# Optimization experiments

Hardware: AMD Instinct MI355X
Metric: run time of the kernel (lower is better)

## Reference

```python
import jax, jax.numpy as jnp
import numpy as np
from jax import lax

D_MODEL = 1024
D_STATE = 1024  # must equal D_MODEL due to u*B elementwise multiply in selective_scan
D_CONV = 4
BATCH = 4
SEQ = 4096


def setup_inputs() -> dict:
    key = jax.random.key(0)
    ks = jax.random.split(key, 12)
    s = 0.02
    return {
        "x": jax.random.normal(ks[0], (BATCH, SEQ, D_MODEL), jnp.float32),
        "ln_g": jnp.ones((D_MODEL,), jnp.float32),
        "ln_b": jnp.zeros((D_MODEL,), jnp.float32),
        "w_in": jax.random.normal(ks[1], (2 * D_MODEL, D_MODEL), jnp.float32) * s,
        "b_in": jnp.zeros((2 * D_MODEL,), jnp.float32),
        "w_conv": jax.random.normal(ks[2], (D_MODEL, 1, D_CONV), jnp.float32) * 0.2,
        "b_conv": jnp.zeros((D_MODEL,), jnp.float32),
        "w_delta": jax.random.normal(ks[3], (D_STATE, D_MODEL), jnp.float32) * s,
        "b_delta": jnp.zeros((D_STATE,), jnp.float32),
        "w_B": jax.random.normal(ks[4], (D_STATE, D_MODEL), jnp.float32) * s,
        "b_B": jnp.zeros((D_STATE,), jnp.float32),
        "w_C": jax.random.normal(ks[5], (D_STATE, D_MODEL), jnp.float32) * s,
        "b_C": jnp.zeros((D_STATE,), jnp.float32),
        "w_out": jax.random.normal(ks[6], (D_MODEL, D_MODEL), jnp.float32) * s,
        "b_out": jnp.zeros((D_MODEL,), jnp.float32),
    }


def reference(x, ln_g, ln_b, w_in, b_in, w_conv, b_conv,
              w_delta, b_delta, w_B, b_B, w_C, b_C, w_out, b_out):
    eps = 1e-5
    # LayerNorm
    mu = jnp.mean(x, axis=-1, keepdims=True)
    var = jnp.mean(jnp.square(x - mu), axis=-1, keepdims=True)
    h = (x - mu) * lax.rsqrt(var + eps) * ln_g + ln_b
    # in_proj and chunk
    uv = h @ w_in.T + b_in  # [B, L, 2D]
    u, v = jnp.split(uv, 2, axis=-1)
    # depthwise causal conv1d: torch pads both sides by K-1 then slices [:L] -> left pad only
    K = w_conv.shape[-1]
    u_c = lax.conv_general_dilated(
        u.transpose(0, 2, 1), w_conv, window_strides=(1,),
        padding=[(K - 1, 0)], feature_group_count=u.shape[-1],
        dimension_numbers=("NCH", "OIH", "NCH"))
    u_c = u_c.transpose(0, 2, 1) + b_conv  # [B, L, D]
    # projections
    delta = jax.nn.softplus(u_c @ w_delta.T + b_delta)  # [B, L, N]
    Bm = u_c @ w_B.T + b_B                              # [B, L, N]
    Cm = u_c @ w_C.T + b_C                              # [B, L, N]
    # selective scan: A = -1 broadcast over d_state
    decay = jnp.exp(-delta)        # exp(delta * A)
    inp = u_c * Bm                 # requires d_model == d_state

    def step(hst, t):
        d_t, i_t, c_t = t
        hst = hst * d_t + i_t
        return hst, jnp.sum(hst * c_t, axis=-1)  # [B]

    h0 = jnp.zeros((x.shape[0], Bm.shape[-1]), x.dtype)
    _, ys = lax.scan(step, h0,
                     (decay.transpose(1, 0, 2), inp.transpose(1, 0, 2), Cm.transpose(1, 0, 2)))
    y = ys.T[..., None]            # [B, L, 1]
    y = y * jax.nn.sigmoid(v)      # broadcast to [B, L, D]
    out = y @ w_out.T + b_out
    return x + out
```

## Files before the change

kernel.cpp:

```cpp
#include <hip/hip_runtime.h>
#include <stdint.h>

#define D_MODEL 1024
#define KDIM 1024
#define BATCH 4
#define SEQ 4096
#define MROWS (BATCH*SEQ)
#define CHUNK 64
#define NCHUNK (SEQ/CHUNK)

typedef unsigned short u16;
typedef __attribute__((ext_vector_type(8))) short short8;
typedef __attribute__((ext_vector_type(4))) float f32x4;
typedef __attribute__((ext_vector_type(4))) unsigned short u16x4;

__device__ __forceinline__ u16 f2bf(float f){
  uint32_t b = __builtin_bit_cast(uint32_t, f);
  b += 0x7FFFu + ((b >> 16) & 1u);
  return (u16)(b >> 16);
}
__device__ __forceinline__ float bf2f(u16 u){
  uint32_t b = ((uint32_t)u) << 16;
  return __builtin_bit_cast(float, b);
}

__global__ __launch_bounds__(256) void prep_ln_kernel(
    const float* __restrict__ w_in, const float* __restrict__ w_delta,
    const float* __restrict__ w_B, const float* __restrict__ w_C,
    const float* __restrict__ w_out,
    const float* __restrict__ b_delta, const float* __restrict__ b_B,
    const float* __restrict__ b_C,
    u16* __restrict__ w_in_bf, u16* __restrict__ wcat_bf,
    u16* __restrict__ w_out_bf, float* __restrict__ bcat,
    const float* __restrict__ x, const float* __restrict__ g,
    const float* __restrict__ bb, u16* __restrict__ h){
  if (blockIdx.x >= 6147){
    int row = blockIdx.x - 6147;
    int tid = threadIdx.x, lane = tid & 63, wid = tid >> 6;
    const float* xr = x + (size_t)row * D_MODEL;
    float4 v = *(const float4*)(xr + tid * 4);
    float s  = v.x + v.y + v.z + v.w;
    float s2 = v.x*v.x + v.y*v.y + v.z*v.z + v.w*v.w;
#pragma unroll
    for (int off = 32; off > 0; off >>= 1){ s += __shfl_down(s, off); s2 += __shfl_down(s2, off); }
    __shared__ float red[8];
    if (lane == 0){ red[wid] = s; red[4 + wid] = s2; }
    __syncthreads();
    s  = red[0] + red[1] + red[2] + red[3];
    s2 = red[4] + red[5] + red[6] + red[7];
    float mu  = s * (1.f / D_MODEL);
    float var = s2 * (1.f / D_MODEL) - mu * mu;
    float rs  = rsqrtf(var + 1e-5f);
    int c = tid * 4;
    u16x4 o;
    o.x = f2bf((v.x - mu) * rs * g[c+0] + bb[c+0]);
    o.y = f2bf((v.y - mu) * rs * g[c+1] + bb[c+1]);
    o.z = f2bf((v.z - mu) * rs * g[c+2] + bb[c+2]);
    o.w = f2bf((v.w - mu) * rs * g[c+3] + bb[c+3]);
    *(u16x4*)(h + (size_t)row * D_MODEL + c) = o;
    return;
  }
  int i4 = blockIdx.x * 256 + threadIdx.x;
  const float* src; u16* dst; int off;
  if      (i4 <  524288){ src = w_in;    dst = w_in_bf;           off = i4; }
  else if (i4 <  786432){ src = w_delta; dst = wcat_bf;           off = i4 -  524288; }
  else if (i4 < 1048576){ src = w_B;     dst = wcat_bf + 1048576; off = i4 -  786432; }
  else if (i4 < 1310720){ src = w_C;     dst = wcat_bf + 2097152; off = i4 - 1048576; }
  else if (i4 < 1572864){ src = w_out;   dst = w_out_bf;          off = i4 - 1310720; }
  else {
    int t = i4 - 1572864;
    if      (t < 256){ *(float4*)(bcat +        t*4)        = *(const float4*)(b_delta + t*4); }
    else if (t < 512){ *(float4*)(bcat + 1024 + (t-256)*4)  = *(const float4*)(b_B + (t-256)*4); }
    else if (t < 768){ *(float4*)(bcat + 2048 + (t-512)*4)  = *(const float4*)(b_C + (t-512)*4); }
    return;
  }
  float4 v = *(const float4*)(src + (size_t)off * 4);
  u16x4 o; o.x = f2bf(v.x); o.y = f2bf(v.y); o.z = f2bf(v.z); o.w = f2bf(v.w);
  *(u16x4*)(dst + (size_t)off * 4) = o;
}

#define VMCNT_(N) asm volatile("s_waitcnt vmcnt(" #N ")" ::: "memory")
#define VMCNT(N) VMCNT_(N)

template<int EPI>
__global__ __launch_bounds__(512, 2) void gemm256(
    const u16* __restrict__ A, const u16* __restrict__ W,
    const float* __restrict__ bias,
    u16* __restrict__ outb, float* __restrict__ outf,
    const float* __restrict__ resid, int N){
  __shared__ char lds[131072];
  const int tid = threadIdx.x, wid = tid >> 6, lane = tid & 63;
  const int wm = wid >> 2, wn = wid & 3;
  const int lrow = lane & 15, khi = lane >> 4;

  int nwg = gridDim.x;
  int cpx = nwg >> 3;
  int bid = blockIdx.x;
  int wg = (bid & 7) * cpx + (bid >> 3);
  int ntile = N >> 8;
  int by = wg / ntile, bx = wg % ntile;
  int m0 = by << 8, n0 = bx << 8;

  f32x4 acc[8][4];
  f32x4 zero = {0.f, 0.f, 0.f, 0.f};
#pragma unroll
  for (int i = 0; i < 8; i++)
#pragma unroll
    for (int j = 0; j < 4; j++) acc[i][j] = zero;

  const int xr = ((lrow >> 1) & 3) << 4;
  const int aOff = (wm * 128 + lrow) * 64 + ((khi * 16) ^ xr);
  const int bOff = (wn * 64  + lrow) * 64 + ((khi * 16) ^ xr);

  const int rS = tid >> 2;
  const int cbS = ((tid & 3) * 16) ^ (((rS >> 1) & 3) << 4);
  const u16* gA = A + (size_t)(m0 + rS) * KDIM + (cbS >> 1);
  const u16* gB = W + (size_t)(n0 + rS) * KDIM + (cbS >> 1);

  auto stA = [&](int kt, int bi){
    const u16* g0 = gA + kt;
    unsigned l0 = (unsigned)(bi * 16384 + wid * 1024);
    __builtin_amdgcn_global_load_lds((const __attribute__((address_space(1))) void*)g0,
                                     (__attribute__((address_space(3))) void*)(lds + l0), 16, 0, 0);
    __builtin_amdgcn_global_load_lds((const __attribute__((address_space(1))) void*)(g0 + 128 * KDIM),
                                     (__attribute__((address_space(3))) void*)(lds + l0 + 8192), 16, 0, 0);
  };
  auto stB = [&](int kt, int bi){
    const u16* g0 = gB + kt;
    unsigned l0 = (unsigned)(65536 + bi * 16384 + wid * 1024);
    __builtin_amdgcn_global_load_lds((const __attribute__((address_space(1))) void*)g0,
                                     (__attribute__((address_space(3))) void*)(lds + l0), 16, 0, 0);
    __builtin_amdgcn_global_load_lds((const __attribute__((address_space(1))) void*)(g0 + 128 * KDIM),
                                     (__attribute__((address_space(3))) void*)(lds + l0 + 8192), 16, 0, 0);
  };

#define TILE(BI, STKT, DOSTAGE, WAITC) { \
  const char* pa = lds + (BI) * 16384; \
  const char* pb = lds + 65536 + (BI) * 16384; \
  short8 bfr[4], afr[8]; \
  _Pragma("unroll") \
  for (int nf = 0; nf < 4; nf++) bfr[nf] = *(const short8*)(pb + bOff + nf * 1024); \
  _Pragma("unroll") \
  for (int mi = 0; mi < 8; mi++) afr[mi] = *(const short8*)(pa + aOff + mi * 1024); \
  if (DOSTAGE){ stA((STKT), ((BI) + 3) & 3); stB((STKT), ((BI) + 3) & 3); } \
  __builtin_amdgcn_sched_barrier(0); \
  __builtin_amdgcn_s_setprio(1); \
  _Pragma("unroll") \
  for (int mi = 0; mi < 8; mi++) \
    _Pragma("unroll") \
    for (int nf = 0; nf < 4; nf++) \
      acc[mi][nf] = __builtin_amdgcn_mfma_f32_16x16x32_bf16(afr[mi], bfr[nf], acc[mi][nf], 0, 0, 0); \
  __builtin_amdgcn_s_setprio(0); \
  WAITC; \
  __builtin_amdgcn_s_barrier(); \
}

  stA(0, 0);  stB(0, 0);
  stA(32, 1); stB(32, 1);
  stA(64, 2); stB(64, 2);
  VMCNT(8);
  __builtin_amdgcn_s_barrier();

  for (int kk = 0; kk < 28; kk += 4){
    TILE(0, (kk + 3) << 5, 1, VMCNT(8));
    TILE(1, (kk + 4) << 5, 1, VMCNT(8));
    TILE(2, (kk + 5) << 5, 1, VMCNT(8));
    TILE(3, (kk + 6) << 5, 1, VMCNT(8));
  }
  TILE(0, 992, 1, VMCNT(8));
  TILE(1, 0, 0, VMCNT(4));
  TILE(2, 0, 0, VMCNT(0));
  TILE(3, 0, 0, (void)0);
#undef TILE

  float bv[4];
#pragma unroll
  for (int nf = 0; nf < 4; nf++) bv[nf] = bias[n0 + wn * 64 + nf * 16 + lrow];
#pragma unroll
  for (int mf = 0; mf < 8; mf++){
    int r0 = m0 + wm * 128 + mf * 16 + khi * 4;
#pragma unroll
    for (int nf = 0; nf < 4; nf++){
      int c = n0 + wn * 64 + nf * 16 + lrow;
#pragma unroll
      for (int i2 = 0; i2 < 4; i2++){
        float val = acc[mf][nf][i2] + bv[nf];
        size_t o = (size_t)(r0 + i2) * N + c;
        if (EPI == 0) outb[o] = f2bf(val);
        else          outf[o] = val + resid[o];
      }
    }
  }
}

__global__ __launch_bounds__(256) void conv_kernel(const u16* __restrict__ uv,
    const float* __restrict__ wc, const float* __restrict__ bc, u16* __restrict__ uc){
  int idx = blockIdx.x * 256 + threadIdx.x;
  int d0 = (idx & 127) * 8;
  int m0 = (idx >> 7) * 16;
  int l0 = m0 & (SEQ - 1);
  float4 wv[8]; float bias[8];
#pragma unroll
  for (int j = 0; j < 8; j++){ wv[j] = *(const float4*)(wc + (d0 + j) * 4); bias[j] = bc[d0 + j]; }
  short8 zero8 = {0,0,0,0,0,0,0,0};
  short8 w0 = zero8, w1 = zero8, w2 = zero8;
  if (l0 > 0){
    w0 = *(const short8*)(uv + (size_t)(m0 - 3) * 2048 + d0);
    w1 = *(const short8*)(uv + (size_t)(m0 - 2) * 2048 + d0);
    w2 = *(const short8*)(uv + (size_t)(m0 - 1) * 2048 + d0);
  }
  const u16* pi = uv + (size_t)m0 * 2048 + d0;
  u16* po = uc + (size_t)m0 * 1024 + d0;
#pragma unroll 4
  for (int t = 0; t < 16; t++){
    short8 cur = *(const short8*)pi;  pi += 2048;
    short8 o;
#pragma unroll
    for (int j = 0; j < 8; j++){
      float a = bias[j] + bf2f((u16)w0[j]) * wv[j].x + bf2f((u16)w1[j]) * wv[j].y
                        + bf2f((u16)w2[j]) * wv[j].z + bf2f((u16)cur[j]) * wv[j].w;
      o[j] = (short)f2bf(a);
    }
    *(short8*)po = o;  po += 1024;
    w0 = w1; w1 = w2; w2 = cur;
  }
}

__global__ __launch_bounds__(256) void scanA(const u16* __restrict__ dbc, const u16* __restrict__ uc,
                                             u16* __restrict__ G, float* __restrict__ P,
                                             float* __restrict__ S, float* __restrict__ ylocal){
  int b = blockIdx.x >> 6, c = blockIdx.x & (NCHUNK - 1);
  int tid = threadIdx.x, n0 = tid * 4;
  __shared__ float part[CHUNK][257];
  __shared__ float red2[CHUNK][5];
  size_t mbase = (size_t)b * SEQ + c * CHUNK;
  float Pv[4] = {1.f,1.f,1.f,1.f}, Sv[4] = {0.f,0.f,0.f,0.f};
  const u16* pd = dbc + mbase * 3072 + n0;
  const u16* pu = uc + mbase * 1024 + n0;
  u16* pg = G + mbase * 1024 + n0;
#pragma unroll 2
  for (int t = 0; t < CHUNK; t++){
    u16x4 dr = *(const u16x4*)pd;
    u16x4 bm = *(const u16x4*)(pd + 1024);
    u16x4 cm = *(const u16x4*)(pd + 2048);
    u16x4 uu = *(const u16x4*)pu;
    pd += 3072; pu += 1024;
    float contrib = 0.f;
    u16x4 go;
#pragma unroll
    for (int j = 0; j < 4; j++){
      float dec = 1.f / (1.f + __expf(bf2f(dr[j])));
      float cf = bf2f(cm[j]);
      Pv[j] *= dec;
      Sv[j] = Sv[j] * dec + bf2f(uu[j]) * bf2f(bm[j]);
      go[j] = f2bf(Pv[j] * cf);
      contrib += Sv[j] * cf;
    }
    *(u16x4*)pg = go;  pg += 1024;
    part[t][tid] = contrib;
  }
  __syncthreads();
  {
    int t = tid & 63, q = tid >> 6;
    float s = 0.f;
#pragma unroll
    for (int j = 0; j < 64; j++) s += part[t][q * 64 + j];
    red2[t][q] = s;
  }
  __syncthreads();
  if (tid < CHUNK)
    ylocal[mbase + tid] = red2[tid][0] + red2[tid][1] + red2[tid][2] + red2[tid][3];
  int o = (b * NCHUNK + c) * 1024 + n0;
  float4 p4 = {Pv[0], Pv[1], Pv[2], Pv[3]};
  float4 s4 = {Sv[0], Sv[1], Sv[2], Sv[3]};
  *(float4*)(P + o) = p4;
  *(float4*)(S + o) = s4;
}

__global__ void scanB(const float* __restrict__ P, const float* __restrict__ S,
                      float* __restrict__ Hin){
  int idx = blockIdx.x * 256 + threadIdx.x;
  int n0 = (idx & 255) * 4, b = idx >> 8;
  float4 H = {0.f,0.f,0.f,0.f};
  for (int c = 0; c < NCHUNK; c++){
    int o = (b * NCHUNK + c) * 1024 + n0;
    *(float4*)(Hin + o) = H;
    float4 p = *(const float4*)(P + o);
    float4 s = *(const float4*)(S + o);
    H.x = H.x * p.x + s.x;  H.y = H.y * p.y + s.y;
    H.z = H.z * p.z + s.z;  H.w = H.w * p.w + s.w;
  }
}

__global__ __launch_bounds__(256) void scanC(u16* gbuf, const float* __restrict__ Hin,
                                             const float* __restrict__ ylocal,
                                             const u16* __restrict__ uv){
  int b = blockIdx.x >> 6, c = blockIdx.x & (NCHUNK - 1);
  int tid = threadIdx.x, n0 = tid * 4;
  __shared__ float part[CHUNK][257];
  __shared__ float red2[CHUNK][5];
  __shared__ float ys[CHUNK];
  size_t mbase = (size_t)b * SEQ + c * CHUNK;
  float4 h4 = *(const float4*)(Hin + (b * NCHUNK + c) * 1024 + n0);
  const u16* pG = gbuf + mbase * 1024 + n0;
#pragma unroll 4
  for (int t = 0; t < CHUNK; t++){
    u16x4 g = *(const u16x4*)pG;  pG += 1024;
    part[t][tid] = h4.x * bf2f(g.x) + h4.y * bf2f(g.y)
                 + h4.z * bf2f(g.z) + h4.w * bf2f(g.w);
  }
  __syncthreads();
  {
    int t = tid & 63, q = tid >> 6;
    float s = 0.f;
#pragma unroll
    for (int j = 0; j < 64; j++) s += part[t][q * 64 + j];
    red2[t][q] = s;
  }
  __syncthreads();
  if (tid < CHUNK)
    ys[tid] = red2[tid][0] + red2[tid][1] + red2[tid][2] + red2[tid][3] + ylocal[mbase + tid];
  __syncthreads();
  const u16* pv = uv + mbase * 2048 + 1024;
  u16* pg = gbuf + mbase * 1024;
#pragma unroll 4
  for (int i2 = 0; i2 < 32; i2++){
    int e = i2 * 256 + tid;
    int t = e >> 7, ch = e & 127;
    short8 v = *(const short8*)(pv + (size_t)t * 2048 + ch * 8);
    float yv = ys[t];
    short8 o;
#pragma unroll
    for (int j = 0; j < 8; j++){
      float vf = bf2f((u16)v[j]);
      float sg = 1.f / (1.f + __expf(-vf));
      o[j] = (short)f2bf(yv * sg);
    }
    *(short8*)(pg + (size_t)t * 1024 + ch * 8) = o;
  }
}

extern "C" void kernel_launch(void* const* d_in, const int* in_sizes, int n_in,
                              void* d_out, int out_size, void* d_ws, size_t ws_size,
                              hipStream_t stream) {
  const float* x      = (const float*)d_in[0];
  const float* ln_g   = (const float*)d_in[1];
  const float* ln_b   = (const float*)d_in[2];
  const float* w_in   = (const float*)d_in[3];
  const float* b_in   = (const float*)d_in[4];
  const float* w_conv = (const float*)d_in[5];
  const float* b_conv = (const float*)d_in[6];
  const float* w_delta= (const float*)d_in[7];
  const float* b_delta= (const float*)d_in[8];
  const float* w_B    = (const float*)d_in[9];
  const float* b_B    = (const float*)d_in[10];
  const float* w_C    = (const float*)d_in[11];
  const float* b_C    = (const float*)d_in[12];
  const float* w_out  = (const float*)d_in[13];
  const float* b_out  = (const float*)d_in[14];

  char* w = (char*)d_ws;
  u16* w_in_bf  = (u16*)w; w += (size_t)2 * 1024 * 1024 * 2;
  u16* wcat_bf  = (u16*)w; w += (size_t)3 * 1024 * 1024 * 2;
  u16* w_out_bf = (u16*)w; w += (size_t)1024 * 1024 * 2;
  float* bcat   = (float*)w; w += 16384;
  u16* h_bf     = (u16*)w; w += (size_t)MROWS * 1024 * 2;
  u16* uv_bf    = (u16*)w; w += (size_t)MROWS * 2048 * 2;
  u16* uc_bf    = (u16*)w; w += (size_t)MROWS * 1024 * 2;
  u16* dbc_bf   = (u16*)w; w += (size_t)MROWS * 3072 * 2;
  float* P      = (float*)w; w += (size_t)BATCH * NCHUNK * 1024 * 4;
  float* S      = (float*)w; w += (size_t)BATCH * NCHUNK * 1024 * 4;
  float* Hin    = (float*)w; w += (size_t)BATCH * NCHUNK * 1024 * 4;
  float* ylocal = (float*)w; w += (size_t)MROWS * 4;
  u16* gbuf     = h_bf;

  prep_ln_kernel<<<6147 + MROWS, 256, 0, stream>>>(
      w_in, w_delta, w_B, w_C, w_out, b_delta, b_B, b_C,
      w_in_bf, wcat_bf, w_out_bf, bcat, x, ln_g, ln_b, h_bf);

  gemm256<0><<<dim3((2048/256) * (MROWS/256)), 512, 0, stream>>>(
      h_bf, w_in_bf, b_in, uv_bf, nullptr, nullptr, 2048);

  conv_kernel<<<(MROWS / 16) * 128 / 256, 256, 0, stream>>>(uv_bf, w_conv, b_conv, uc_bf);

  gemm256<0><<<dim3((3072/256) * (MROWS/256)), 512, 0, stream>>>(
      uc_bf, wcat_bf, bcat, dbc_bf, nullptr, nullptr, 3072);

  scanA<<<BATCH * NCHUNK, 256, 0, stream>>>(dbc_bf, uc_bf, gbuf, P, S, ylocal);
  scanB<<<(BATCH * 1024 / 4) / 256, 256, 0, stream>>>(P, S, Hin);
  scanC<<<BATCH * NCHUNK, 256, 0, stream>>>(gbuf, Hin, ylocal, uv_bf);

  gemm256<1><<<dim3((1024/256) * (MROWS/256)), 512, 0, stream>>>(
      gbuf, w_out_bf, b_out, nullptr, (float*)d_out, x, 1024);
}
```

Before: 333.1 us.

## Factor per-row scan output out of out_proj GEMM and fuse sigmoid into in_proj

Since y is a per-row scalar, y*sigmoid(v) @ W_out^T equals y * (sigmoid(v) @ W_out^T). The sigmoid is now applied in the in_proj GEMM epilogue to the v half. The out GEMM reads sigmoid(v) straight from uv_bf with stride 2048 and scales each row by y in its epilogue. This removes scanC's gating pass, which read v and wrote a full bf16 gated tensor. The cost is a strided A operand in the out GEMM and a few extra sigmoid evaluations in the first GEMM epilogue.

```diff
diff --git a/kernel.cpp b/kernel.cpp
--- a/kernel.cpp
+++ b/kernel.cpp
@@ -82,12 +82,13 @@
 #define VMCNT_(N) asm volatile("s_waitcnt vmcnt(" #N ")" ::: "memory")
 #define VMCNT(N) VMCNT_(N)
 
-template<int EPI>
+template<int EPI, int SIG>
 __global__ __launch_bounds__(512, 2) void gemm256(
     const u16* __restrict__ A, const u16* __restrict__ W,
     const float* __restrict__ bias,
     u16* __restrict__ outb, float* __restrict__ outf,
-    const float* __restrict__ resid, int N){
+    const float* __restrict__ resid, const float* __restrict__ yv,
+    int N, int lda){
   __shared__ char lds[131072];
   const int tid = threadIdx.x, wid = tid >> 6, lane = tid & 63;
   const int wm = wid >> 2, wn = wid & 3;
@@ -114,7 +115,7 @@
 
   const int rS = tid >> 2;
   const int cbS = ((tid & 3) * 16) ^ (((rS >> 1) & 3) << 4);
-  const u16* gA = A + (size_t)(m0 + rS) * KDIM + (cbS >> 1);
+  const u16* gA = A + (size_t)(m0 + rS) * lda + (cbS >> 1);
   const u16* gB = W + (size_t)(n0 + rS) * KDIM + (cbS >> 1);
 
   auto stA = [&](int kt, int bi){
@@ -122,7 +123,7 @@
     unsigned l0 = (unsigned)(bi * 16384 + wid * 1024);
     __builtin_amdgcn_global_load_lds((const __attribute__((address_space(1))) void*)g0,
                                      (__attribute__((address_space(3))) void*)(lds + l0), 16, 0, 0);
-    __builtin_amdgcn_global_load_lds((const __attribute__((address_space(1))) void*)(g0 + 128 * KDIM),
+    __builtin_amdgcn_global_load_lds((const __attribute__((address_space(1))) void*)(g0 + (size_t)128 * lda),
                                      (__attribute__((address_space(3))) void*)(lds + l0 + 8192), 16, 0, 0);
   };
   auto stB = [&](int kt, int bi){
@@ -176,6 +177,7 @@
   float bv[4];
 #pragma unroll
   for (int nf = 0; nf < 4; nf++) bv[nf] = bias[n0 + wn * 64 + nf * 16 + lrow];
+  const bool dosig = SIG && (n0 >= 1024);
 #pragma unroll
   for (int mf = 0; mf < 8; mf++){
     int r0 = m0 + wm * 128 + mf * 16 + khi * 4;
@@ -186,8 +188,13 @@
       for (int i2 = 0; i2 < 4; i2++){
         float val = acc[mf][nf][i2] + bv[nf];
         size_t o = (size_t)(r0 + i2) * N + c;
-        if (EPI == 0) outb[o] = f2bf(val);
-        else          outf[o] = val + resid[o];
+        if (EPI == 0){
+          if (SIG && dosig) val = 1.f / (1.f + __expf(-val));
+          outb[o] = f2bf(val);
+        } else {
+          float yrow = yv[r0 + i2];
+          outf[o] = acc[mf][nf][i2] * yrow + bv[nf] + resid[o];
+        }
       }
     }
   }
@@ -292,17 +299,15 @@
   }
 }
 
-__global__ __launch_bounds__(256) void scanC(u16* gbuf, const float* __restrict__ Hin,
-                                             const float* __restrict__ ylocal,
-                                             const u16* __restrict__ uv){
+__global__ __launch_bounds__(256) void scanC(const u16* __restrict__ G, const float* __restrict__ Hin,
+                                             const float* __restrict__ ylocal, float* __restrict__ ysg){
   int b = blockIdx.x >> 6, c = blockIdx.x & (NCHUNK - 1);
   int tid = threadIdx.x, n0 = tid * 4;
   __shared__ float part[CHUNK][257];
   __shared__ float red2[CHUNK][5];
-  __shared__ float ys[CHUNK];
   size_t mbase = (size_t)b * SEQ + c * CHUNK;
   float4 h4 = *(const float4*)(Hin + (b * NCHUNK + c) * 1024 + n0);
-  const u16* pG = gbuf + mbase * 1024 + n0;
+  const u16* pG = G + mbase * 1024 + n0;
 #pragma unroll 4
   for (int t = 0; t < CHUNK; t++){
     u16x4 g = *(const u16x4*)pG;  pG += 1024;
@@ -319,25 +324,8 @@
   }
   __syncthreads();
   if (tid < CHUNK)
-    ys[tid] = red2[tid][0] + red2[tid][1] + red2[tid][2] + red2[tid][3] + ylocal[mbase + tid];
-  __syncthreads();
-  const u16* pv = uv + mbase * 2048 + 1024;
-  u16* pg = gbuf + mbase * 1024;
-#pragma unroll 4
-  for (int i2 = 0; i2 < 32; i2++){
-    int e = i2 * 256 + tid;
-    int t = e >> 7, ch = e & 127;
-    short8 v = *(const short8*)(pv + (size_t)t * 2048 + ch * 8);
-    float yv = ys[t];
-    short8 o;
-#pragma unroll
-    for (int j = 0; j < 8; j++){
-      float vf = bf2f((u16)v[j]);
-      float sg = 1.f / (1.f + __expf(-vf));
-      o[j] = (short)f2bf(yv * sg);
-    }
-    *(short8*)(pg + (size_t)t * 1024 + ch * 8) = o;
-  }
+    ysg[mbase + tid] = red2[tid][0] + red2[tid][1] + red2[tid][2] + red2[tid][3]
+                     + ylocal[mbase + tid];
 }
 
 extern "C" void kernel_launch(void* const* d_in, const int* in_sizes, int n_in,
@@ -372,24 +360,25 @@
   float* S      = (float*)w; w += (size_t)BATCH * NCHUNK * 1024 * 4;
   float* Hin    = (float*)w; w += (size_t)BATCH * NCHUNK * 1024 * 4;
   float* ylocal = (float*)w; w += (size_t)MROWS * 4;
+  float* ysg    = (float*)w; w += (size_t)MROWS * 4;
   u16* gbuf     = h_bf;
 
   prep_ln_kernel<<<6147 + MROWS, 256, 0, stream>>>(
       w_in, w_delta, w_B, w_C, w_out, b_delta, b_B, b_C,
       w_in_bf, wcat_bf, w_out_bf, bcat, x, ln_g, ln_b, h_bf);
 
-  gemm256<0><<<dim3((2048/256) * (MROWS/256)), 512, 0, stream>>>(
-      h_bf, w_in_bf, b_in, uv_bf, nullptr, nullptr, 2048);
+  gemm256<0,1><<<dim3((2048/256) * (MROWS/256)), 512, 0, stream>>>(
+      h_bf, w_in_bf, b_in, uv_bf, nullptr, nullptr, nullptr, 2048, 1024);
 
   conv_kernel<<<(MROWS / 16) * 128 / 256, 256, 0, stream>>>(uv_bf, w_conv, b_conv, uc_bf);
 
-  gemm256<0><<<dim3((3072/256) * (MROWS/256)), 512, 0, stream>>>(
-      uc_bf, wcat_bf, bcat, dbc_bf, nullptr, nullptr, 3072);
+  gemm256<0,0><<<dim3((3072/256) * (MROWS/256)), 512, 0, stream>>>(
+      uc_bf, wcat_bf, bcat, dbc_bf, nullptr, nullptr, nullptr, 3072, 1024);
 
   scanA<<<BATCH * NCHUNK, 256, 0, stream>>>(dbc_bf, uc_bf, gbuf, P, S, ylocal);
   scanB<<<(BATCH * 1024 / 4) / 256, 256, 0, stream>>>(P, S, Hin);
-  scanC<<<BATCH * NCHUNK, 256, 0, stream>>>(gbuf, Hin, ylocal, uv_bf);
-
-  gemm256<1><<<dim3((1024/256) * (MROWS/256)), 512, 0, stream>>>(
-      gbuf, w_out_bf, b_out, nullptr, (float*)d_out, x, 1024);
-}
+  scanC<<<BATCH * NCHUNK, 256, 0, stream>>>(gbuf, Hin, ylocal, ysg);
+
+  gemm256<1,0><<<dim3((1024/256) * (MROWS/256)), 512, 0, stream>>>(
+      uv_bf + 1024, w_out_bf, b_out, nullptr, (float*)d_out, x, ysg, 1024, 2048);
+}
```

Result: faster. 321.0 us (-3.6%).
